# Performance work log

Hardware: AMD Instinct MI355X
Metric: run time of the kernel (lower is better)

Reference implementation:

```python
import jax, jax.numpy as jnp
import numpy as np

DIM = 192
WIN = (8, 8)
NUM_HEADS = 6
HEAD_DIM = DIM // NUM_HEADS
SCALE = HEAD_DIM ** -0.5
N = WIN[0] * WIN[1]
NUM_REL = (2 * WIN[0] - 1) * (2 * WIN[1] - 1)


def make_rel_pos_index():
    h = np.arange(WIN[0]); w = np.arange(WIN[1])
    idx = np.stack(np.meshgrid(w, h, indexing='ij')).reshape(2, -1)  # (2, N)
    rel = idx[:, :, None] - idx[:, None, :]                          # (2, N, N)
    rel = np.transpose(rel, (1, 2, 0)).copy()
    rel[:, :, 0] += WIN[0] - 1
    rel[:, :, 1] += WIN[1] - 1
    rel[:, :, 0] *= 2 * WIN[1] - 1
    return np.sum(rel, -1)  # (N, N) int indices into bias table

REL_POS_INDEX = make_rel_pos_index()


def setup_inputs() -> dict:
    key = jax.random.key(0)
    ks = jax.random.split(key, 8)
    B = 2048   # num_windows_per_image (64) * images (32)
    nW = 64
    inputs = jax.random.normal(ks[0], (B, N, DIM), dtype=jnp.float32)
    mask = jax.random.normal(ks[1], (nW, N, N), dtype=jnp.float32)
    w_qkv = jax.random.normal(ks[2], (DIM, 3 * DIM), dtype=jnp.float32) * (DIM ** -0.5)
    b_qkv = jnp.zeros((3 * DIM,), dtype=jnp.float32)
    rpbt = jax.random.normal(ks[3], (NUM_REL, NUM_HEADS), dtype=jnp.float32) * 0.02
    w_proj = jax.random.normal(ks[4], (DIM, DIM), dtype=jnp.float32) * (DIM ** -0.5)
    b_proj = jnp.zeros((DIM,), dtype=jnp.float32)
    return {"inputs": inputs, "mask": mask, "w_qkv": w_qkv, "b_qkv": b_qkv,
            "rpbt": rpbt, "w_proj": w_proj, "b_proj": b_proj}


def reference(inputs, mask, w_qkv, b_qkv, rpbt, w_proj, b_proj):
    batch, n, channels = inputs.shape
    qkv = inputs @ w_qkv + b_qkv                                   # (B, n, 3C)
    qkv = qkv.reshape(batch, n, 3, NUM_HEADS, channels // NUM_HEADS)
    qkv = jnp.transpose(qkv, (2, 0, 3, 1, 4))                      # (3, B, H, n, d)
    q, k, v = qkv[0], qkv[1], qkv[2]
    att = jnp.einsum('bhnd,bhmd->bhnm', q * SCALE, k)              # (B, H, n, n)
    # gather relative position bias: (n, n, H) -> (H, n, n)
    rel_bias = rpbt[REL_POS_INDEX.reshape(-1)].reshape(n, n, NUM_HEADS)
    att = att + jnp.transpose(rel_bias, (2, 0, 1))[None]
    nW = mask.shape[0]
    att = att.reshape(batch // nW, nW, NUM_HEADS, n, n)
    att = att + mask[None, :, None]
    att = att.reshape(-1, NUM_HEADS, n, n)
    att = jax.nn.softmax(att, axis=-1)
    x = jnp.einsum('bhnm,bhmd->bnhd', att, v).reshape(batch, n, channels)
    return x @ w_proj + b_proj
```

## Files before the change

### kernel.cpp

```cpp
#include <hip/hip_runtime.h>
#include <hip/hip_bf16.h>
#include <cstdint>


#define NTOK 64
#define NH 6
#define HD 32
#define WDIM 192
#define SCALE 0.17677669529663689f

typedef __bf16 bf16x8 __attribute__((ext_vector_type(8)));
typedef float f32x4 __attribute__((ext_vector_type(4)));

__device__ inline unsigned short f2bf(float f) {
    union { float f; unsigned u; } v; v.f = f;
    unsigned r = v.u + 0x7fff + ((v.u >> 16) & 1);
    return (unsigned short)(r >> 16);
}

__global__ __launch_bounds__(256) void prep_kernel(
    const float* __restrict__ w_qkv, const float* __restrict__ w_proj,
    const float* __restrict__ rpbt, const float* __restrict__ mask,
    unsigned short* __restrict__ wqkv_f, unsigned short* __restrict__ wproj_f,
    float* __restrict__ comb) {
    int idx = blockIdx.x * 256 + threadIdx.x;
    if (idx < 576 * 192) {
        int j = idx & 7, lane = (idx >> 3) & 63, t = idx >> 9;
        int ks = t % 6, ntile = t / 6;
        int n = ntile * 16 + (lane & 15);
        int k = ks * 32 + (lane >> 4) * 8 + j;
        wqkv_f[idx] = f2bf(w_qkv[k * 576 + n]);
        return;
    }
    int i2 = idx - 576 * 192;
    if (i2 < 192 * 192) {
        int j = i2 & 7, lane = (i2 >> 3) & 63, t = i2 >> 9;
        int ks = t % 6, ntile = t / 6;
        int n = ntile * 16 + (lane & 15);
        int k = ks * 32 + (lane >> 4) * 8 + j;
        wproj_f[i2] = f2bf(w_proj[k * 192 + n]);
        return;
    }
    int i3 = i2 - 192 * 192;
    if (i3 < 64 * NH * NTOK * NTOK) {
        int c = i3 & 63, r = (i3 >> 6) & 63;
        int h = (i3 >> 12) % NH;
        int w = i3 / (NH * 4096);
        int rr = (r >> 3) - (c >> 3) + 7;
        int cc = (r & 7) - (c & 7) + 7;
        comb[i3] = rpbt[(rr * 15 + cc) * NH + h] + mask[w * 4096 + r * 64 + c];
    }
}

__global__ __launch_bounds__(512, 2) void fused_kernel(
    const float* __restrict__ X, const unsigned short* __restrict__ Wqf,
    const float* __restrict__ b_qkv, const unsigned short* __restrict__ Wpf,
    const float* __restrict__ b_proj, const float* __restrict__ comb,
    float* __restrict__ out) {
    __shared__ unsigned short sm[19456];
    unsigned short* lx   = sm;
    unsigned short* lq2  = sm;
    unsigned short* lk2  = sm + 5120;
    unsigned short* lvt2 = sm + 10240;
    unsigned short* lxa  = sm + 14848;

    const int tid = threadIdx.x;
    const int bwin = blockIdx.x;
    const int wave = tid >> 6, lane = tid & 63;
    const int l15 = lane & 15, quad = lane >> 4;
    const int wm = wave >> 2, wn = wave & 3;

    const float4* xg = (const float4*)(X + (size_t)bwin * 64 * 192);
    for (int i = 0; i < 6; i++) {
        int e4 = tid + i * 512;
        int row = e4 / 48, c4 = e4 % 48;
        float4 v = xg[e4];
        union { unsigned short s[4]; uint2 u; } pk;
        pk.s[0] = f2bf(v.x); pk.s[1] = f2bf(v.y);
        pk.s[2] = f2bf(v.z); pk.s[3] = f2bf(v.w);
        *(uint2*)&lx[row * 200 + c4 * 4] = pk.u;
    }
    __syncthreads();

    bf16x8 af[2][6];
    for (int mt = 0; mt < 2; mt++)
        for (int ks = 0; ks < 6; ks++)
            af[mt][ks] = *(const bf16x8*)&lx[(wm * 32 + mt * 16 + l15) * 200 + ks * 32 + quad * 8];
    unsigned short* lspw = sm + wave * 1152;

    f32x4 pacc[2][3];
    for (int mt = 0; mt < 2; mt++)
        for (int nt = 0; nt < 3; nt++)
            pacc[mt][nt] = (f32x4){0.f, 0.f, 0.f, 0.f};

    const float* combg = comb + ((size_t)(bwin & 63) * NH) * 4096;

    for (int p = 0; p < 3; p++) {
        f32x4 acc[2][3];
        for (int mt = 0; mt < 2; mt++)
            for (int i = 0; i < 3; i++)
                acc[mt][i] = (f32x4){0.f, 0.f, 0.f, 0.f};
        for (int ks = 0; ks < 6; ks++) {
            bf16x8 bfr[3];
            for (int i = 0; i < 3; i++) {
                int f = wn * 3 + i, c = f >> 2, j = f & 3;
                bfr[i] = *(const bf16x8*)&Wqf[
                    ((size_t)((c * 12 + p * 4 + j) * 6 + ks)) * 512 + lane * 8];
            }
            for (int mt = 0; mt < 2; mt++)
                for (int i = 0; i < 3; i++)
                    acc[mt][i] = __builtin_amdgcn_mfma_f32_16x16x32_bf16(
                        af[mt][ks], bfr[i], acc[mt][i], 0, 0, 0);
        }
        __syncthreads();
        for (int i = 0; i < 3; i++) {
            int f = wn * 3 + i, c = f >> 2, j = f & 3;
            int cw = j * 16 + l15;
            float bias = b_qkv[c * 192 + p * 64 + cw];
            int hl = cw >> 5, d = cw & 31;
            if (c < 2) {
                unsigned short* dst = (c == 0) ? lq2 : lk2;
                for (int mt = 0; mt < 2; mt++)
                    for (int r = 0; r < 4; r++) {
                        int t = wm * 32 + mt * 16 + quad * 4 + r;
                        dst[(hl * 64 + t) * 40 + d] = f2bf(acc[mt][i][r] + bias);
                    }
            } else {
                for (int mt = 0; mt < 2; mt++) {
                    union { unsigned short s[4]; uint2 u; } pk;
                    for (int r = 0; r < 4; r++)
                        pk.s[r] = f2bf(acc[mt][i][r] + bias);
                    int t0 = wm * 32 + mt * 16 + quad * 4;
                    *(uint2*)&lvt2[(hl * 32 + d) * 72 + t0] = pk.u;
                }
            }
        }
        __syncthreads();

        const int hl = wm;
        const int mbase = wn * 16;
        const int hg = p * 2 + hl;

        float cmb[4][4];
        for (int j = 0; j < 4; j++)
            for (int r = 0; r < 4; r++)
                cmb[j][r] = combg[hg * 4096 + (mbase + quad * 4 + r) * 64 + j * 16 + l15];

        bf16x8 aq = *(const bf16x8*)&lq2[(hl * 64 + mbase + l15) * 40 + quad * 8];
        f32x4 sacc[4];
        for (int j = 0; j < 4; j++) {
            bf16x8 bk = *(const bf16x8*)&lk2[(hl * 64 + j * 16 + l15) * 40 + quad * 8];
            f32x4 z = (f32x4){0.f, 0.f, 0.f, 0.f};
            sacc[j] = __builtin_amdgcn_mfma_f32_16x16x32_bf16(aq, bk, z, 0, 0, 0);
        }
        __syncthreads();

        float pr[4][4], rsum[4];
        for (int r = 0; r < 4; r++) {
            float s0 = sacc[0][r] * SCALE + cmb[0][r];
            float s1 = sacc[1][r] * SCALE + cmb[1][r];
            float s2 = sacc[2][r] * SCALE + cmb[2][r];
            float s3 = sacc[3][r] * SCALE + cmb[3][r];
            float m = fmaxf(fmaxf(s0, s1), fmaxf(s2, s3));
            for (int o = 1; o < 16; o <<= 1) m = fmaxf(m, __shfl_xor(m, o, 64));
            pr[0][r] = __expf(s0 - m); pr[1][r] = __expf(s1 - m);
            pr[2][r] = __expf(s2 - m); pr[3][r] = __expf(s3 - m);
            float su = pr[0][r] + pr[1][r] + pr[2][r] + pr[3][r];
            for (int o = 1; o < 16; o <<= 1) su += __shfl_xor(su, o, 64);
            rsum[r] = su;
        }

        for (int j = 0; j < 4; j++)
            for (int r = 0; r < 4; r++)
                lspw[(quad * 4 + r) * 72 + j * 16 + l15] = f2bf(pr[j][r]);

        f32x4 oacc[2];
        oacc[0] = (f32x4){0.f, 0.f, 0.f, 0.f};
        oacc[1] = (f32x4){0.f, 0.f, 0.f, 0.f};
        for (int kstep = 0; kstep < 2; kstep++) {
            bf16x8 ap = *(const bf16x8*)&lspw[l15 * 72 + kstep * 32 + quad * 8];
            for (int n2 = 0; n2 < 2; n2++) {
                bf16x8 bv = *(const bf16x8*)&lvt2[
                    (hl * 32 + n2 * 16 + l15) * 72 + kstep * 32 + quad * 8];
                oacc[n2] = __builtin_amdgcn_mfma_f32_16x16x32_bf16(ap, bv, oacc[n2], 0, 0, 0);
            }
        }

        for (int r = 0; r < 4; r++) {
            float inv = 1.0f / rsum[r];
            int t = mbase + quad * 4 + r;
            for (int n2 = 0; n2 < 2; n2++)
                lxa[t * 72 + hl * 32 + n2 * 16 + l15] = f2bf(oacc[n2][r] * inv);
        }
        __syncthreads();

        bf16x8 pf[2][2];
        for (int mt = 0; mt < 2; mt++)
            for (int kk = 0; kk < 2; kk++)
                pf[mt][kk] = *(const bf16x8*)&lxa[
                    (wm * 32 + mt * 16 + l15) * 72 + kk * 32 + quad * 8];
        for (int kk = 0; kk < 2; kk++) {
            bf16x8 bfr[3];
            for (int nt = 0; nt < 3; nt++)
                bfr[nt] = *(const bf16x8*)&Wpf[
                    ((size_t)((wn * 3 + nt) * 6 + (p * 2 + kk))) * 512 + lane * 8];
            for (int mt = 0; mt < 2; mt++)
                for (int nt = 0; nt < 3; nt++)
                    pacc[mt][nt] = __builtin_amdgcn_mfma_f32_16x16x32_bf16(
                        pf[mt][kk], bfr[nt], pacc[mt][nt], 0, 0, 0);
        }
    }

    for (int nt = 0; nt < 3; nt++) {
        int cw = wn * 48 + nt * 16 + l15;
        float bias = b_proj[cw];
        for (int mt = 0; mt < 2; mt++)
            for (int r = 0; r < 4; r++) {
                int t = wm * 32 + mt * 16 + quad * 4 + r;
                out[((size_t)bwin * 64 + t) * 192 + cw] = pacc[mt][nt][r] + bias;
            }
    }
}

extern "C" void kernel_launch(void* const* d_in, const int* in_sizes, int n_in,
                              void* d_out, int out_size, void* d_ws, size_t ws_size,
                              hipStream_t stream) {
    const float* x      = (const float*)d_in[0];
    const float* mask   = (const float*)d_in[1];
    const float* w_qkv  = (const float*)d_in[2];
    const float* b_qkv  = (const float*)d_in[3];
    const float* rpbt   = (const float*)d_in[4];
    const float* w_proj = (const float*)d_in[5];
    const float* b_proj = (const float*)d_in[6];
    float* out = (float*)d_out;

    const int B = in_sizes[0] / (NTOK * WDIM);

    char* ws = (char*)d_ws;
    size_t o = 0;
    unsigned short* Wq = (unsigned short*)(ws + o); o += 576 * 192 * 2;
    unsigned short* Wp = (unsigned short*)(ws + o); o += 192 * 192 * 2;
    float* comb        = (float*)(ws + o);         o += (size_t)64 * NH * NTOK * NTOK * 4;

    const int prep_elems = 576 * 192 + 192 * 192 + 64 * NH * NTOK * NTOK;
    prep_kernel<<<(prep_elems + 255) / 256, 256, 0, stream>>>(
        w_qkv, w_proj, rpbt, mask, Wq, Wp, comb);
    fused_kernel<<<B, 512, 0, stream>>>(
        x, Wq, b_qkv, Wp, b_proj, comb, out);
}
```

Measured before the change: 298.5 us.

## Prefetch weights, hoist bias loads, and drop a barrier via separate softmax LDS

Moves the per-wave softmax scratch buffer into its own LDS region so the barrier after the QK^T MFMAs can be removed. Issues the combined bias/mask global loads at the top of each head-pair iteration and double-buffers the QKV weight fragments across k-steps, so global latency overlaps with MFMA work. The projection weights are also loaded before the attention-output barrier. The bf16 conversion switches to the hardware cast and the loops are fully unrolled. LDS use grows to about 56 KB per block, which may limit occupancy at two blocks per CU and raises register pressure.

```diff
diff --git a/kernel.cpp b/kernel.cpp
--- a/kernel.cpp
+++ b/kernel.cpp
@@ -13,9 +13,9 @@
 typedef float f32x4 __attribute__((ext_vector_type(4)));
 
 __device__ inline unsigned short f2bf(float f) {
-    union { float f; unsigned u; } v; v.f = f;
-    unsigned r = v.u + 0x7fff + ((v.u >> 16) & 1);
-    return (unsigned short)(r >> 16);
+    union { __bf16 b; unsigned short s; } u;
+    u.b = (__bf16)f;
+    return u.s;
 }
 
 __global__ __launch_bounds__(256) void prep_kernel(
@@ -57,7 +57,7 @@
     const float* __restrict__ b_qkv, const unsigned short* __restrict__ Wpf,
     const float* __restrict__ b_proj, const float* __restrict__ comb,
     float* __restrict__ out) {
-    __shared__ unsigned short sm[19456];
+    __shared__ unsigned short sm[28672];
     unsigned short* lx   = sm;
     unsigned short* lq2  = sm;
     unsigned short* lk2  = sm + 5120;
@@ -86,7 +86,7 @@
     for (int mt = 0; mt < 2; mt++)
         for (int ks = 0; ks < 6; ks++)
             af[mt][ks] = *(const bf16x8*)&lx[(wm * 32 + mt * 16 + l15) * 200 + ks * 32 + quad * 8];
-    unsigned short* lspw = sm + wave * 1152;
+    unsigned short* lspw = sm + 19456 + wave * 1152;
 
     f32x4 pacc[2][3];
     for (int mt = 0; mt < 2; mt++)
@@ -96,66 +96,92 @@
     const float* combg = comb + ((size_t)(bwin & 63) * NH) * 4096;
 
     for (int p = 0; p < 3; p++) {
+        const int hl = wm;
+        const int mbase = wn * 16;
+        const int hg = p * 2 + hl;
+
+        float cmb[4][4];
+        #pragma unroll
+        for (int j = 0; j < 4; j++)
+            #pragma unroll
+            for (int r = 0; r < 4; r++)
+                cmb[j][r] = combg[hg * 4096 + (mbase + quad * 4 + r) * 64 + j * 16 + l15];
+
+        const unsigned short* wptr[3];
+        #pragma unroll
+        for (int i = 0; i < 3; i++) {
+            int f = wn * 3 + i, c = f >> 2, j = f & 3;
+            wptr[i] = Wqf + ((size_t)((c * 12 + p * 4 + j) * 6)) * 512 + lane * 8;
+        }
         f32x4 acc[2][3];
-        for (int mt = 0; mt < 2; mt++)
+        #pragma unroll
+        for (int mt = 0; mt < 2; mt++)
+            #pragma unroll
             for (int i = 0; i < 3; i++)
                 acc[mt][i] = (f32x4){0.f, 0.f, 0.f, 0.f};
+
+        bf16x8 bcur[3], bnxt[3];
+        #pragma unroll
+        for (int i = 0; i < 3; i++)
+            bcur[i] = *(const bf16x8*)(wptr[i]);
+        #pragma unroll
         for (int ks = 0; ks < 6; ks++) {
-            bf16x8 bfr[3];
-            for (int i = 0; i < 3; i++) {
-                int f = wn * 3 + i, c = f >> 2, j = f & 3;
-                bfr[i] = *(const bf16x8*)&Wqf[
-                    ((size_t)((c * 12 + p * 4 + j) * 6 + ks)) * 512 + lane * 8];
-            }
+            if (ks < 5) {
+                #pragma unroll
+                for (int i = 0; i < 3; i++)
+                    bnxt[i] = *(const bf16x8*)(wptr[i] + (ks + 1) * 512);
+            }
+            #pragma unroll
             for (int mt = 0; mt < 2; mt++)
+                #pragma unroll
                 for (int i = 0; i < 3; i++)
                     acc[mt][i] = __builtin_amdgcn_mfma_f32_16x16x32_bf16(
-                        af[mt][ks], bfr[i], acc[mt][i], 0, 0, 0);
+                        af[mt][ks], bcur[i], acc[mt][i], 0, 0, 0);
+            #pragma unroll
+            for (int i = 0; i < 3; i++)
+                bcur[i] = bnxt[i];
         }
         __syncthreads();
+        #pragma unroll
         for (int i = 0; i < 3; i++) {
             int f = wn * 3 + i, c = f >> 2, j = f & 3;
             int cw = j * 16 + l15;
             float bias = b_qkv[c * 192 + p * 64 + cw];
-            int hl = cw >> 5, d = cw & 31;
+            int hle = cw >> 5, d = cw & 31;
             if (c < 2) {
                 unsigned short* dst = (c == 0) ? lq2 : lk2;
+                #pragma unroll
                 for (int mt = 0; mt < 2; mt++)
+                    #pragma unroll
                     for (int r = 0; r < 4; r++) {
                         int t = wm * 32 + mt * 16 + quad * 4 + r;
-                        dst[(hl * 64 + t) * 40 + d] = f2bf(acc[mt][i][r] + bias);
+                        dst[(hle * 64 + t) * 40 + d] = f2bf(acc[mt][i][r] + bias);
                     }
             } else {
+                #pragma unroll
                 for (int mt = 0; mt < 2; mt++) {
                     union { unsigned short s[4]; uint2 u; } pk;
+                    #pragma unroll
                     for (int r = 0; r < 4; r++)
                         pk.s[r] = f2bf(acc[mt][i][r] + bias);
                     int t0 = wm * 32 + mt * 16 + quad * 4;
-                    *(uint2*)&lvt2[(hl * 32 + d) * 72 + t0] = pk.u;
+                    *(uint2*)&lvt2[(hle * 32 + d) * 72 + t0] = pk.u;
                 }
             }
         }
         __syncthreads();
-
-        const int hl = wm;
-        const int mbase = wn * 16;
-        const int hg = p * 2 + hl;
-
-        float cmb[4][4];
-        for (int j = 0; j < 4; j++)
-            for (int r = 0; r < 4; r++)
-                cmb[j][r] = combg[hg * 4096 + (mbase + quad * 4 + r) * 64 + j * 16 + l15];
 
         bf16x8 aq = *(const bf16x8*)&lq2[(hl * 64 + mbase + l15) * 40 + quad * 8];
         f32x4 sacc[4];
+        #pragma unroll
         for (int j = 0; j < 4; j++) {
             bf16x8 bk = *(const bf16x8*)&lk2[(hl * 64 + j * 16 + l15) * 40 + quad * 8];
             f32x4 z = (f32x4){0.f, 0.f, 0.f, 0.f};
             sacc[j] = __builtin_amdgcn_mfma_f32_16x16x32_bf16(aq, bk, z, 0, 0, 0);
         }
-        __syncthreads();
 
         float pr[4][4], rsum[4];
+        #pragma unroll
         for (int r = 0; r < 4; r++) {
             float s0 = sacc[0][r] * SCALE + cmb[0][r];
             float s1 = sacc[1][r] * SCALE + cmb[1][r];
@@ -170,15 +196,19 @@
             rsum[r] = su;
         }
 
+        #pragma unroll
         for (int j = 0; j < 4; j++)
+            #pragma unroll
             for (int r = 0; r < 4; r++)
                 lspw[(quad * 4 + r) * 72 + j * 16 + l15] = f2bf(pr[j][r]);
 
         f32x4 oacc[2];
         oacc[0] = (f32x4){0.f, 0.f, 0.f, 0.f};
         oacc[1] = (f32x4){0.f, 0.f, 0.f, 0.f};
+        #pragma unroll
         for (int kstep = 0; kstep < 2; kstep++) {
             bf16x8 ap = *(const bf16x8*)&lspw[l15 * 72 + kstep * 32 + quad * 8];
+            #pragma unroll
             for (int n2 = 0; n2 < 2; n2++) {
                 bf16x8 bv = *(const bf16x8*)&lvt2[
                     (hl * 32 + n2 * 16 + l15) * 72 + kstep * 32 + quad * 8];
@@ -186,29 +216,46 @@
             }
         }
 
+        bf16x8 pb0[3];
+        #pragma unroll
+        for (int nt = 0; nt < 3; nt++)
+            pb0[nt] = *(const bf16x8*)&Wpf[
+                ((size_t)((wn * 3 + nt) * 6 + (p * 2 + 0))) * 512 + lane * 8];
+
+        #pragma unroll
         for (int r = 0; r < 4; r++) {
             float inv = 1.0f / rsum[r];
             int t = mbase + quad * 4 + r;
+            #pragma unroll
             for (int n2 = 0; n2 < 2; n2++)
                 lxa[t * 72 + hl * 32 + n2 * 16 + l15] = f2bf(oacc[n2][r] * inv);
         }
         __syncthreads();
 
+        bf16x8 pb1[3];
+        #pragma unroll
+        for (int nt = 0; nt < 3; nt++)
+            pb1[nt] = *(const bf16x8*)&Wpf[
+                ((size_t)((wn * 3 + nt) * 6 + (p * 2 + 1))) * 512 + lane * 8];
         bf16x8 pf[2][2];
-        for (int mt = 0; mt < 2; mt++)
+        #pragma unroll
+        for (int mt = 0; mt < 2; mt++)
+            #pragma unroll
             for (int kk = 0; kk < 2; kk++)
                 pf[mt][kk] = *(const bf16x8*)&lxa[
                     (wm * 32 + mt * 16 + l15) * 72 + kk * 32 + quad * 8];
-        for (int kk = 0; kk < 2; kk++) {
-            bf16x8 bfr[3];
+        #pragma unroll
+        for (int mt = 0; mt < 2; mt++)
+            #pragma unroll
             for (int nt = 0; nt < 3; nt++)
-                bfr[nt] = *(const bf16x8*)&Wpf[
-                    ((size_t)((wn * 3 + nt) * 6 + (p * 2 + kk))) * 512 + lane * 8];
-            for (int mt = 0; mt < 2; mt++)
-                for (int nt = 0; nt < 3; nt++)
-                    pacc[mt][nt] = __builtin_amdgcn_mfma_f32_16x16x32_bf16(
-                        pf[mt][kk], bfr[nt], pacc[mt][nt], 0, 0, 0);
-        }
+                pacc[mt][nt] = __builtin_amdgcn_mfma_f32_16x16x32_bf16(
+                    pf[mt][0], pb0[nt], pacc[mt][nt], 0, 0, 0);
+        #pragma unroll
+        for (int mt = 0; mt < 2; mt++)
+            #pragma unroll
+            for (int nt = 0; nt < 3; nt++)
+                pacc[mt][nt] = __builtin_amdgcn_mfma_f32_16x16x32_bf16(
+                    pf[mt][1], pb1[nt], pacc[mt][nt], 0, 0, 0);
     }
 
     for (int nt = 0; nt < 3; nt++) {
```

Result: faster. 291.4 us (-2.4%).
